# Kernel optimization log

Hardware: AMD Instinct MI355X
Metric: run time of the kernel (lower is better)

The kernel has to match this reference:

```python
import jax, jax.numpy as jnp
import numpy as np

CHANNELS = 256
BATCH, H, W = 32, 56, 56
K = 26  # round(256 * 0.1)
BOOST_STRENGTH = 1.0


def setup_inputs() -> dict:
    key = jax.random.key(0)
    k1, k2 = jax.random.split(key)
    x = jax.random.normal(k1, (BATCH, CHANNELS, H, W), dtype=jnp.float32)
    duty_cycle = jax.random.uniform(k2, (1, CHANNELS, 1, 1), dtype=jnp.float32)
    return {"x": x, "duty_cycle": duty_cycle, "k": K,
            "boost_strength": jnp.float32(BOOST_STRENGTH)}


def reference(x, duty_cycle, k, boost_strength):
    # boost_activations: x.detach() * exp(-boost_strength * duty_cycle)
    # (boost_strength > 0 in this configuration)
    boosted = jax.lax.stop_gradient(x) * jnp.exp(-boost_strength * duty_cycle)
    # local kwinners: per (b,h,w) location, kthvalue over channels at index
    # C - k + 1 (1-based ascending) == k-th largest boosted value.
    C = x.shape[1]
    sorted_b = jnp.sort(boosted, axis=1)           # ascending over channels
    threshold = sorted_b[:, C - k:C - k + 1, :, :]  # [B,1,H,W], k-th largest
    # off_mask = boosted < threshold; masked_fill with 0 keeps boosted >= threshold
    keep = boosted >= threshold
    return jnp.where(keep, x, jnp.zeros((), dtype=x.dtype))
```

## Files before the change

### kernel.cpp

```cpp
#include <hip/hip_runtime.h>
#include <math.h>

#define C_CH 256
#define KTOP 26
#define HWSZ 3136
#define NPIX 100352
#define CHW  (C_CH * HWSZ)
#define PIX_PER_BLK 64
#define CPT 32

__device__ __forceinline__ void ce_desc(float& a, float& b) {
    float mx = fmaxf(a, b); float mn = fminf(a, b); a = mx; b = mn;
}
__device__ __forceinline__ void ce_asc(float& a, float& b) {
    float mn = fminf(a, b); float mx = fmaxf(a, b); a = mn; b = mx;
}

__device__ __forceinline__ void sort32_desc(float* v) {
#pragma unroll
    for (int k = 2; k <= 32; k <<= 1) {
#pragma unroll
        for (int j = k >> 1; j > 0; j >>= 1) {
#pragma unroll
            for (int i = 0; i < 32; ++i) {
                int l = i ^ j;
                if (l > i) {
                    if ((i & k) == 0) ce_desc(v[i], v[l]);
                    else              ce_asc(v[i], v[l]);
                }
            }
        }
    }
}

__device__ __forceinline__ void clean32_desc(float* v) {
#pragma unroll
    for (int j = 16; j > 0; j >>= 1) {
#pragma unroll
        for (int i = 0; i < 32; ++i) {
            int l = i ^ j;
            if (l > i) ce_desc(v[i], v[l]);
        }
    }
}

__device__ __forceinline__ void merge26(float* a, const float* __restrict__ src) {
    float h[32];
#pragma unroll
    for (int i = 0; i < 32; ++i) {
        float u = (i < KTOP)      ? a[i]        : -INFINITY;
        float w = (31 - i < KTOP) ? src[31 - i] : -INFINITY;
        h[i] = fmaxf(u, w);
    }
    clean32_desc(h);
#pragma unroll
    for (int j = 0; j < KTOP; ++j) a[j] = h[j];
}

__global__ __launch_bounds__(512, 4) void kwinners_kernel(
    const float* __restrict__ x, const float* __restrict__ duty,
    const float* __restrict__ bsp, float* __restrict__ out)
{
    __shared__ float s[C_CH];
    __shared__ float lbuf[4][PIX_PER_BLK][27];
    __shared__ float thr_lds[PIX_PER_BLK];

    const int t = threadIdx.x;
    if (t < C_CH) {
        float bs = bsp[0];
        float m = -(bs * duty[t]);
        s[t] = (float)exp((double)m);
    }
    __syncthreads();

    const int w   = t >> 6;
    const int pl  = t & 63;
    const int blk = blockIdx.x;
    const int b   = blk / 49;
    const int hw  = (blk - b * 49) * 64 + pl;
    const int c0  = w * CPT;

    const float* xp = x   + (size_t)b * CHW + (size_t)c0 * HWSZ + hw;
    float*       op = out + (size_t)b * CHW + (size_t)c0 * HWSZ + hw;
    const float* sc = s + c0;

    float o[CPT];
#pragma unroll
    for (int i = 0; i < CPT; ++i) o[i] = xp[(size_t)i * HWSZ];

    float v[CPT];
#pragma unroll
    for (int i = 0; i < CPT; ++i) v[i] = o[i] * sc[i];

    sort32_desc(v);

    if (w & 1) {
        float* dst = lbuf[w >> 1][pl];
#pragma unroll
        for (int j = 0; j < KTOP; ++j) dst[j] = v[j];
    }
    __syncthreads();

    if (!(w & 1)) {
        merge26(v, lbuf[w >> 1][pl]);
        if (w == 2 || w == 6) {
            float* dst = lbuf[w >> 1][pl];
#pragma unroll
            for (int j = 0; j < KTOP; ++j) dst[j] = v[j];
        }
    }
    __syncthreads();

    if (w == 0 || w == 4) {
        merge26(v, lbuf[(w >> 1) + 1][pl]);
        if (w == 4) {
            float* dst = lbuf[2][pl];
#pragma unroll
            for (int j = 0; j < KTOP; ++j) dst[j] = v[j];
        }
    }
    __syncthreads();

    if (w == 0) {
        const float* src = lbuf[2][pl];
        float h[32];
#pragma unroll
        for (int i = 0; i < 32; ++i) {
            float u = (i < KTOP)      ? v[i]        : -INFINITY;
            float wv = (31 - i < KTOP) ? src[31 - i] : -INFINITY;
            h[i] = fmaxf(u, wv);
        }
        float l16[16];
#pragma unroll
        for (int i = 0; i < 16; ++i) l16[i] = fminf(h[i], h[i + 16]);
        float l8[8];
#pragma unroll
        for (int i = 0; i < 8; ++i)  l8[i]  = fminf(l16[i], l16[i + 8]);
        float h4[4];
#pragma unroll
        for (int i = 0; i < 4; ++i)  h4[i]  = fmaxf(l8[i], l8[i + 4]);
        float h2[2];
#pragma unroll
        for (int i = 0; i < 2; ++i)  h2[i]  = fmaxf(h4[i], h4[i + 2]);
        thr_lds[pl] = fminf(h2[0], h2[1]);
    }
    __syncthreads();

    const float thr = thr_lds[pl];

#pragma unroll
    for (int i = 0; i < CPT; ++i) {
        float bv = o[i] * sc[i];
        op[(size_t)i * HWSZ] = (bv >= thr) ? o[i] : 0.0f;
    }
}

extern "C" void kernel_launch(void* const* d_in, const int* in_sizes, int n_in,
                              void* d_out, int out_size, void* d_ws, size_t ws_size,
                              hipStream_t stream) {
    const float* x    = (const float*)d_in[0];
    const float* duty = (const float*)d_in[1];
    const float* bs   = (const float*)d_in[3];
    float* out = (float*)d_out;

    hipLaunchKernelGGL(kwinners_kernel, dim3(NPIX / PIX_PER_BLK), dim3(512), 0,
                       stream, x, duty, bs, out);
}
```

Baseline: 44.15 us.

## Split channels into 16 groups per pixel with cross-half shuffle merge

Each block now handles 32 pixels instead of 64, with each thread holding 16 channels instead of 32. The two half-waves merge their sorted lists through a __shfl_xor, and the rest of the top-26 merge tree is restructured to three serial merges per reducing wave. The goals are lower register pressure (launch bounds raised to 5 blocks per CU), a cheaper per-thread sort, and twice as many blocks. In exchange, each wave's global accesses cover only 32 contiguous pixels (128B segments), and the serial merges in waves 0 and 4 lengthen the critical path.

```diff
diff --git a/kernel.cpp b/kernel.cpp
--- a/kernel.cpp
+++ b/kernel.cpp
@@ -6,8 +6,9 @@
 #define HWSZ 3136
 #define NPIX 100352
 #define CHW  (C_CH * HWSZ)
-#define PIX_PER_BLK 64
-#define CPT 32
+#define PIX_PER_BLK 32
+#define BLKS_PER_IMG 98
+#define CPT 16
 
 __device__ __forceinline__ void ce_desc(float& a, float& b) {
     float mx = fmaxf(a, b); float mn = fminf(a, b); a = mx; b = mn;
@@ -16,13 +17,13 @@
     float mn = fminf(a, b); float mx = fmaxf(a, b); a = mn; b = mx;
 }
 
-__device__ __forceinline__ void sort32_desc(float* v) {
+__device__ __forceinline__ void sort16_desc(float* v) {
 #pragma unroll
-    for (int k = 2; k <= 32; k <<= 1) {
+    for (int k = 2; k <= 16; k <<= 1) {
 #pragma unroll
         for (int j = k >> 1; j > 0; j >>= 1) {
 #pragma unroll
-            for (int i = 0; i < 32; ++i) {
+            for (int i = 0; i < 16; ++i) {
                 int l = i ^ j;
                 if (l > i) {
                     if ((i & k) == 0) ce_desc(v[i], v[l]);
@@ -57,12 +58,12 @@
     for (int j = 0; j < KTOP; ++j) a[j] = h[j];
 }
 
-__global__ __launch_bounds__(512, 4) void kwinners_kernel(
+__global__ __launch_bounds__(512, 5) void kwinners_kernel(
     const float* __restrict__ x, const float* __restrict__ duty,
     const float* __restrict__ bsp, float* __restrict__ out)
 {
     __shared__ float s[C_CH];
-    __shared__ float lbuf[4][PIX_PER_BLK][27];
+    __shared__ float lbuf[6][PIX_PER_BLK][27];
     __shared__ float thr_lds[PIX_PER_BLK];
 
     const int t = threadIdx.x;
@@ -74,15 +75,18 @@
     __syncthreads();
 
     const int w   = t >> 6;
-    const int pl  = t & 63;
+    const int l   = t & 63;
+    const int pl  = l & 31;
+    const int sub = l >> 5;
+    const int g   = 2 * w + sub;
     const int blk = blockIdx.x;
-    const int b   = blk / 49;
-    const int hw  = (blk - b * 49) * 64 + pl;
-    const int c0  = w * CPT;
+    const int b   = blk / BLKS_PER_IMG;
+    const int hw  = (blk - b * BLKS_PER_IMG) * PIX_PER_BLK + pl;
 
-    const float* xp = x   + (size_t)b * CHW + (size_t)c0 * HWSZ + hw;
-    float*       op = out + (size_t)b * CHW + (size_t)c0 * HWSZ + hw;
-    const float* sc = s + c0;
+    const size_t base = (size_t)b * CHW + (size_t)g * CPT * HWSZ + hw;
+    const float* xp = x + base;
+    float*       op = out + base;
+    const float* sc = s + g * CPT;
 
     float o[CPT];
 #pragma unroll
@@ -92,41 +96,49 @@
 #pragma unroll
     for (int i = 0; i < CPT; ++i) v[i] = o[i] * sc[i];
 
-    sort32_desc(v);
+    sort16_desc(v);
 
-    if (w & 1) {
-        float* dst = lbuf[w >> 1][pl];
+    float a[KTOP];
+    {
+        float h[32];
 #pragma unroll
-        for (int j = 0; j < KTOP; ++j) dst[j] = v[j];
+        for (int j = 0; j < CPT; ++j) h[j] = v[j];
+#pragma unroll
+        for (int j = 0; j < CPT; ++j) h[16 + j] = __shfl_xor(v[15 - j], 32);
+        clean32_desc(h);
+#pragma unroll
+        for (int j = 0; j < KTOP; ++j) a[j] = h[j];
     }
-    __syncthreads();
 
-    if (!(w & 1)) {
-        merge26(v, lbuf[w >> 1][pl]);
-        if (w == 2 || w == 6) {
-            float* dst = lbuf[w >> 1][pl];
+    if (w != 0 && w != 4) {
+        int idx = (w < 4) ? (w - 1) : (w - 2);
+        if (l < 32) {
+            float* dst = lbuf[idx][pl];
 #pragma unroll
-            for (int j = 0; j < KTOP; ++j) dst[j] = v[j];
+            for (int j = 0; j < KTOP; ++j) dst[j] = a[j];
         }
     }
     __syncthreads();
 
     if (w == 0 || w == 4) {
-        merge26(v, lbuf[(w >> 1) + 1][pl]);
-        if (w == 4) {
-            float* dst = lbuf[2][pl];
+        const int o0 = (w == 0) ? 0 : 3;
+        merge26(a, lbuf[o0][pl]);
+        merge26(a, lbuf[o0 + 1][pl]);
+        merge26(a, lbuf[o0 + 2][pl]);
+        if (w == 4 && l < 32) {
+            float* dst = lbuf[3][pl];
 #pragma unroll
-            for (int j = 0; j < KTOP; ++j) dst[j] = v[j];
+            for (int j = 0; j < KTOP; ++j) dst[j] = a[j];
         }
     }
     __syncthreads();
 
     if (w == 0) {
-        const float* src = lbuf[2][pl];
+        const float* src = lbuf[3][pl];
         float h[32];
 #pragma unroll
         for (int i = 0; i < 32; ++i) {
-            float u = (i < KTOP)      ? v[i]        : -INFINITY;
+            float u  = (i < KTOP)      ? a[i]        : -INFINITY;
             float wv = (31 - i < KTOP) ? src[31 - i] : -INFINITY;
             h[i] = fmaxf(u, wv);
         }
@@ -142,7 +154,7 @@
         float h2[2];
 #pragma unroll
         for (int i = 0; i < 2; ++i)  h2[i]  = fmaxf(h4[i], h4[i + 2]);
-        thr_lds[pl] = fminf(h2[0], h2[1]);
+        if (l < 32) thr_lds[pl] = fminf(h2[0], h2[1]);
     }
     __syncthreads();
 
```

New measurement: 55.74 us. +26.3%, slower.
